# Optimization experiments

Measured on AMD Instinct MI355X. Metric: run time of the kernel, lower is better.

## Reference

```python
import jax, jax.numpy as jnp
import numpy as np

U, I, D = 50000, 100000, 64
N = U + I
B = 8192
E_UI = 1_000_000   # directed user->item edges, symmetrized to 2M
E_U = 500_000      # per user metapath graph
E_I = 1_000_000    # per item metapath graph
SA_HID = 128


def _seg_sum(data, idx, n):
    return jax.ops.segment_sum(data, idx, num_segments=n)


def gcn_spmm(edges, x):
    """scipy-style symmetric normalization: D^-1/2 A D^-1/2 x, inf->0."""
    n = x.shape[0]
    row, col = edges[0], edges[1]
    deg = _seg_sum(jnp.ones(row.shape, x.dtype), row, n)  # symmetric adj
    dinv = jnp.where(deg > 0, 1.0 / jnp.sqrt(jnp.maximum(deg, 1e-12)), 0.0)
    msg = x[col] * dinv[col][:, None]          # [E, D] gather
    return _seg_sum(msg, row, n) * dinv[:, None]


def graph_conv(edges, x):
    """DGL GraphConv(norm='both', weight=None, bias=None): degrees clamped min 1."""
    n = x.shape[0]
    src, dst = edges[0], edges[1]
    ones = jnp.ones(src.shape, x.dtype)
    dout = jnp.maximum(_seg_sum(ones, src, n), 1.0)
    din = jnp.maximum(_seg_sum(ones, dst, n), 1.0)
    msg = x[src] * (1.0 / jnp.sqrt(dout))[src][:, None]
    return _seg_sum(msg, dst, n) * (1.0 / jnp.sqrt(din))[:, None]


def han_layer(x, e1, e2, W1, b1, w2):
    # per-metapath GraphConv, stack -> [N, M=2, D]
    z = jnp.stack([graph_conv(e1, x), graph_conv(e2, x)], axis=1)
    w = jnp.tanh(z @ W1 + b1) @ w2            # [N, 2, 1]
    beta = jax.nn.softmax(w.mean(0), axis=0)  # [2, 1]
    return (beta[None, :, :] * z).sum(1)      # [N, D]


def setup_inputs() -> dict:
    key = jax.random.key(0)
    ks = jax.random.split(key, 16)
    user_feat = jax.random.normal(ks[0], (U, D), jnp.float32) * 0.1
    item_feat = jax.random.normal(ks[1], (I, D), jnp.float32) * 0.1
    sa_u_W1 = jax.random.normal(ks[2], (D, SA_HID), jnp.float32) * (1.0 / np.sqrt(D))
    sa_u_b1 = jnp.zeros((SA_HID,), jnp.float32)
    sa_u_w2 = jax.random.normal(ks[3], (SA_HID, 1), jnp.float32) * (1.0 / np.sqrt(SA_HID))
    sa_i_W1 = jax.random.normal(ks[4], (D, SA_HID), jnp.float32) * (1.0 / np.sqrt(D))
    sa_i_b1 = jnp.zeros((SA_HID,), jnp.float32)
    sa_i_w2 = jax.random.normal(ks[5], (SA_HID, 1), jnp.float32) * (1.0 / np.sqrt(SA_HID))
    # symmetric bipartite user-item adjacency over N global nodes
    r = jax.random.randint(ks[6], (E_UI,), 0, U, jnp.int32)
    c = jax.random.randint(ks[7], (E_UI,), U, N, jnp.int32)
    ui_edges = jnp.stack([jnp.concatenate([r, c]), jnp.concatenate([c, r])])  # [2, 2E]
    u_edges1 = jax.random.randint(ks[8], (2, E_U), 0, U, jnp.int32)
    u_edges2 = jax.random.randint(ks[9], (2, E_U), 0, U, jnp.int32)
    i_edges1 = jax.random.randint(ks[10], (2, E_I), 0, I, jnp.int32)
    i_edges2 = jax.random.randint(ks[11], (2, E_I), 0, I, jnp.int32)
    user_idx = jax.random.randint(ks[12], (B,), 0, U, jnp.int32)
    item_idx = jax.random.randint(ks[13], (B,), 0, I, jnp.int32)
    neg_item_idx = jax.random.randint(ks[14], (B,), 0, B, jnp.int32)
    return dict(user_feat=user_feat, item_feat=item_feat,
                sa_u_W1=sa_u_W1, sa_u_b1=sa_u_b1, sa_u_w2=sa_u_w2,
                sa_i_W1=sa_i_W1, sa_i_b1=sa_i_b1, sa_i_w2=sa_i_w2,
                ui_edges=ui_edges, u_edges1=u_edges1, u_edges2=u_edges2,
                i_edges1=i_edges1, i_edges2=i_edges2,
                user_idx=user_idx, item_idx=item_idx, neg_item_idx=neg_item_idx)


def reference(user_feat, item_feat, sa_u_W1, sa_u_b1, sa_u_w2,
              sa_i_W1, sa_i_b1, sa_i_w2, ui_edges, u_edges1, u_edges2,
              i_edges1, i_edges2, user_idx, item_idx, neg_item_idx):
    ui = jnp.concatenate([user_feat, item_feat], axis=0)  # [N, D]
    hu, hi = user_feat, item_feat
    for _ in range(2):
        ui = gcn_spmm(ui_edges, ui)
        hu = han_layer(hu, u_edges1, u_edges2, sa_u_W1, sa_u_b1, sa_u_w2)
        hi = han_layer(hi, i_edges1, i_edges2, sa_i_W1, sa_i_b1, sa_i_w2)
    user_all = 0.5 * hu + 0.5 * ui[:U]
    item_all = 0.5 * hi + 0.5 * ui[U:]
    user_emb = user_all[user_idx]
    item_emb = item_all[item_idx]
    neg_item_feat = item_emb[neg_item_idx]
    return (user_emb, item_emb, neg_item_feat)
```

## Files before the change

kernel.cpp:

```cpp
#include <hip/hip_runtime.h>
#include <hip/hip_bf16.h>
#include <stdint.h>

typedef long long ll;
typedef unsigned short ushort_t;
typedef __attribute__((ext_vector_type(8))) short bf16x8;
typedef __attribute__((ext_vector_type(4))) float f32x4;

static inline int cdiv_ll(ll a, ll b) { return (int)((a + b - 1) / b); }

#define BIN_SHIFT 8
#define BIN_SIZE 256
#define KMAX 3072
#define BT 1024
#define FILL_CAP 7936

__global__ void k_detect(const unsigned int* __restrict__ dw, const ll n_dw, int* __restrict__ flag) {
    __shared__ int sc[256];
    int tid = threadIdx.x;
    int cnt = 0;
    for (int s = 0; s < 32; s++) {
        ll idx = (ll)(s * 256 + tid);
        ll i = (idx * n_dw) / 8192;
        unsigned v = dw[i];
        unsigned lo = v & 0xFFFFu;
        unsigned ex = (lo >> 7) & 0xFFu;
        bool pl = (lo == 0u) || (lo == 0x8000u) || (ex >= 0x60u && ex <= 0x8Fu);
        cnt += pl ? 1 : 0;
    }
    sc[tid] = cnt;
    __syncthreads();
    for (int o = 128; o > 0; o >>= 1) { if (tid < o) sc[tid] += sc[tid + o]; __syncthreads(); }
    if (tid == 0) *flag = (sc[0] * 2 > 8192) ? 1 : 0;
}

__device__ __forceinline__ float load_in(const void* p, ll i, int isbf16) {
    if (isbf16) return __bfloat162float(((const __hip_bfloat16*)p)[i]);
    return ((const float*)p)[i];
}

__device__ __forceinline__ float bf2f(ushort_t u) {
    return __uint_as_float(((unsigned)u) << 16);
}
__device__ __forceinline__ ushort_t f2bf(float f) {
    unsigned u = __float_as_uint(f);
    unsigned r = (u + 0x7FFFu + ((u >> 16) & 1u)) >> 16;
    return (ushort_t)r;
}

__global__ void k_cvt_weights(const void* __restrict__ W1u, const void* __restrict__ b1u,
                              const void* __restrict__ w2u, const void* __restrict__ W1i,
                              const void* __restrict__ b1i, const void* __restrict__ w2i,
                              ushort_t* __restrict__ Wbu, float* __restrict__ fb1u,
                              float* __restrict__ fw2u, ushort_t* __restrict__ Wbi,
                              float* __restrict__ fb1i, float* __restrict__ fw2i,
                              const int* __restrict__ flag) {
    int i = blockIdx.x * blockDim.x + threadIdx.x;
    int bf = *flag;
    const int WSZ = 64 * 128;
    if (i < WSZ) {
        int d = i >> 7, h = i & 127;
        Wbu[h * 64 + d] = f2bf(load_in(W1u, i, bf));
    } else if (i < WSZ + 128) {
        fb1u[i - WSZ] = load_in(b1u, i - WSZ, bf);
    } else if (i < WSZ + 256) {
        fw2u[i - WSZ - 128] = load_in(w2u, i - WSZ - 128, bf);
    } else if (i < 2 * WSZ + 256) {
        int j = i - WSZ - 256;
        int d = j >> 7, h = j & 127;
        Wbi[h * 64 + d] = f2bf(load_in(W1i, j, bf));
    } else if (i < 2 * WSZ + 384) {
        fb1i[i - 2 * WSZ - 256] = load_in(b1i, i - 2 * WSZ - 256, bf);
    } else if (i < 2 * WSZ + 512) {
        fw2i[i - 2 * WSZ - 384] = load_in(w2i, i - 2 * WSZ - 384, bf);
    }
}

__device__ __forceinline__ void decode_rec(ll t,
    const int* __restrict__ uiR, const int* __restrict__ uiC,
    const int* __restrict__ u1s, const int* __restrict__ u1d,
    const int* __restrict__ u2s, const int* __restrict__ u2d,
    const int* __restrict__ i1s, const int* __restrict__ i1d,
    const int* __restrict__ i2s, const int* __restrict__ i2d,
    const ll E2, const ll EU1, const ll EU2, const ll EI1, const ll EI2,
    const int N, const int U, const int I, const int M,
    int& key, int& col) {
    if (t < E2) { key = uiR[t]; col = uiC[t]; return; }
    t -= E2;
    if (t < EU1) { key = N + u1d[t]; col = u1s[t]; return; }
    t -= EU1;
    if (t < EU1) { key = M + u1s[t]; col = 0; return; }
    t -= EU1;
    if (t < EU2) { key = N + U + u2d[t]; col = u2s[t]; return; }
    t -= EU2;
    if (t < EU2) { key = M + U + u2s[t]; col = 0; return; }
    t -= EU2;
    if (t < EI1) { key = N + 2 * U + i1d[t]; col = i1s[t]; return; }
    t -= EI1;
    if (t < EI1) { key = M + 2 * U + i1s[t]; col = 0; return; }
    t -= EI1;
    if (t < EI2) { key = N + 2 * U + I + i2d[t]; col = i2s[t]; return; }
    t -= EI2;
    key = M + 2 * U + I + i2s[t]; col = 0;
}

__device__ __forceinline__ int decode_key(ll t,
    const int* __restrict__ uiR,
    const int* __restrict__ u1s, const int* __restrict__ u1d,
    const int* __restrict__ u2s, const int* __restrict__ u2d,
    const int* __restrict__ i1s, const int* __restrict__ i1d,
    const int* __restrict__ i2s, const int* __restrict__ i2d,
    const ll E2, const ll EU1, const ll EU2, const ll EI1, const ll EI2,
    const int N, const int U, const int I, const int M) {
    if (t < E2) return uiR[t];
    t -= E2;
    if (t < EU1) return N + u1d[t];
    t -= EU1;
    if (t < EU1) return M + u1s[t];
    t -= EU1;
    if (t < EU2) return N + U + u2d[t];
    t -= EU2;
    if (t < EU2) return M + U + u2s[t];
    t -= EU2;
    if (t < EI1) return N + 2 * U + i1d[t];
    t -= EI1;
    if (t < EI1) return M + 2 * U + i1s[t];
    t -= EI1;
    if (t < EI2) return N + 2 * U + I + i2d[t];
    t -= EI2;
    return M + 2 * U + I + i2s[t];
}

#define DECODE_ARGS uiR, uiC, u1s, u1d, u2s, u2d, i1s, i1d, i2s, i2d, \
                    E2, EU1, EU2, EI1, EI2, N, U, I, M

__global__ __launch_bounds__(BT) void kA_hist(
    const int* __restrict__ uiR,
    const int* __restrict__ u1s, const int* __restrict__ u1d,
    const int* __restrict__ u2s, const int* __restrict__ u2d,
    const int* __restrict__ i1s, const int* __restrict__ i1d,
    const int* __restrict__ i2s, const int* __restrict__ i2d,
    const ll E2, const ll EU1, const ll EU2, const ll EI1, const ll EI2,
    const int N, const int U, const int I, const int M,
    const ll RT, const ll CHUNKD, const int K,
    int* __restrict__ btot ,
    int* __restrict__ whist ) {
    __shared__ int hist[KMAX];
    for (int i = threadIdx.x; i < K; i += BT) hist[i] = 0;
    __syncthreads();
    ll base = (ll)blockIdx.x * CHUNKD;
    ll lim = base + CHUNKD;
    if (lim > RT) lim = RT;
    for (ll t = base + threadIdx.x; t < lim; t += BT) {
        int key = decode_key(t, uiR, u1s, u1d, u2s, u2d, i1s, i1d, i2s, i2d,
                             E2, EU1, EU2, EI1, EI2, N, U, I, M);
        atomicAdd(&hist[key >> BIN_SHIFT], 1);
    }
    __syncthreads();
    ll wb = (ll)blockIdx.x * K;
    for (int k = threadIdx.x; k < K; k += BT) {
        int h = hist[k];
        whist[wb + k] = h;
        if (h) atomicAdd(&btot[k * 32], h);
    }
}

__global__ __launch_bounds__(1024) void k_bscan(const int* __restrict__ btot,
                                                int* __restrict__ bbase,
                                                int* __restrict__ bcursor, const int K) {
    __shared__ int sh[1024];
    __shared__ int carry;
    int t = threadIdx.x;
    if (t == 0) carry = 0;
    __syncthreads();
    for (int base = 0; base < K; base += 1024) {
        int idx = base + t;
        int v = (idx < K) ? btot[idx * 32] : 0;
        sh[t] = v;
        __syncthreads();
        for (int off = 1; off < 1024; off <<= 1) {
            int x = (t >= off) ? sh[t - off] : 0;
            __syncthreads();
            sh[t] += x;
            __syncthreads();
        }
        if (idx < K) {
            int ex = carry + sh[t] - v;
            bbase[idx] = ex;
            bcursor[idx * 32] = ex;
        }
        __syncthreads();
        if (t == 0) carry += sh[1023];
        __syncthreads();
    }
}

__global__ __launch_bounds__(BT) void kA_scatter(
    const int* __restrict__ uiR, const int* __restrict__ uiC,
    const int* __restrict__ u1s, const int* __restrict__ u1d,
    const int* __restrict__ u2s, const int* __restrict__ u2d,
    const int* __restrict__ i1s, const int* __restrict__ i1d,
    const int* __restrict__ i2s, const int* __restrict__ i2d,
    const ll E2, const ll EU1, const ll EU2, const ll EI1, const ll EI2,
    const int N, const int U, const int I, const int M,
    const ll RT, const ll CHUNKD, const int K, int* __restrict__ bcursor,
    const int* __restrict__ whist,
    unsigned* __restrict__ binned) {
    __shared__ int lcur[KMAX];
    ll wb = (ll)blockIdx.x * K;
    for (int k = threadIdx.x; k < K; k += BT) {
        int h = whist[wb + k];
        lcur[k] = h ? atomicAdd(&bcursor[k * 32], h) : 0;
    }
    __syncthreads();
    ll base = (ll)blockIdx.x * CHUNKD;
    ll lim = base + CHUNKD;
    if (lim > RT) lim = RT;
    for (ll t = base + threadIdx.x; t < lim; t += BT) {
        int key, col;
        decode_rec(t, DECODE_ARGS, key, col);
        int pos = atomicAdd(&lcur[key >> BIN_SHIFT], 1);
        binned[pos] = ((unsigned)(key & 255) << 24) | (unsigned)col;
    }
}

__global__ __launch_bounds__(256) void kB1_count(const unsigned* __restrict__ binned,
                                                 const int* __restrict__ bbase,
                                                 const int* __restrict__ btot,
                                                 int* __restrict__ counts, const int M2) {
    __shared__ int cnt[BIN_SIZE];
    int b = blockIdx.x;
    int lo = b << BIN_SHIFT;
    int hi = min(lo + BIN_SIZE, M2);
    for (int i = threadIdx.x; i < BIN_SIZE; i += 256) cnt[i] = 0;
    __syncthreads();
    int s = bbase[b], n = btot[b * 32];
    for (int j = s + threadIdx.x; j < s + n; j += 256) {
        atomicAdd(&cnt[binned[j] >> 24], 1);
    }
    __syncthreads();
    for (int i = threadIdx.x; i < hi - lo; i += 256) counts[lo + i] = cnt[i];
}

__global__ void k_norm_all(const int* __restrict__ counts, float* __restrict__ nrm,
                           const int N, const int total) {
    int i = blockIdx.x * blockDim.x + threadIdx.x;
    if (i < total) {
        int c = counts[i];
        if (i < N) nrm[i] = (c > 0) ? (1.0f / sqrtf((float)c)) : 0.0f;
        else nrm[i] = 1.0f / sqrtf(fmaxf((float)c, 1.0f));
    }
}

#define SCAN_T 256
#define SCAN_ELEMS 8
#define SCAN_CHUNK (SCAN_T * SCAN_ELEMS)

__global__ __launch_bounds__(256) void k_scanA(const int* __restrict__ in, const int n,
                                               int* __restrict__ out, int* __restrict__ bsum) {
    __shared__ int sh[SCAN_T];
    int t = threadIdx.x;
    ll base = (ll)blockIdx.x * SCAN_CHUNK + (ll)t * SCAN_ELEMS;
    int v[SCAN_ELEMS];
    int tot = 0;
#pragma unroll
    for (int k = 0; k < SCAN_ELEMS; k++) {
        ll i = base + k;
        v[k] = (i < n) ? in[i] : 0;
        tot += v[k];
    }
    sh[t] = tot;
    __syncthreads();
    for (int off = 1; off < SCAN_T; off <<= 1) {
        int x = (t >= off) ? sh[t - off] : 0;
        __syncthreads();
        sh[t] += x;
        __syncthreads();
    }
    int run = sh[t] - tot;
#pragma unroll
    for (int k = 0; k < SCAN_ELEMS; k++) {
        ll i = base + k;
        if (i < n) out[i] = run;
        run += v[k];
    }
    if (t == SCAN_T - 1) bsum[blockIdx.x] = sh[SCAN_T - 1];
}

__global__ __launch_bounds__(256) void k_scanB(int* __restrict__ bsum, const int nb) {
    __shared__ int sh[256];
    int t = threadIdx.x;
    int running = 0;
    for (int base = 0; base < nb; base += 256) {
        int idx = base + t;
        int v = (idx < nb) ? bsum[idx] : 0;
        sh[t] = v;
        __syncthreads();
        for (int off = 1; off < 256; off <<= 1) {
            int x = (t >= off) ? sh[t - off] : 0;
            __syncthreads();
            sh[t] += x;
            __syncthreads();
        }
        if (idx < nb) bsum[idx] = running + sh[t] - v;
        int tot = sh[255];
        __syncthreads();
        running += tot;
    }
}

__global__ void k_scanC(int* __restrict__ S, const int n, const int* __restrict__ bsum, const int ET) {
    ll i = (ll)blockIdx.x * blockDim.x + threadIdx.x;
    if (i < n) S[i] += bsum[i / SCAN_CHUNK];
    if (i == 0) S[n] = ET;
}

__global__ __launch_bounds__(256) void kB2_fill(const unsigned* __restrict__ binned,
                                                const int* __restrict__ bbase,
                                                const int* __restrict__ btot,
                                                const int* __restrict__ S,
                                                const float* __restrict__ nrm,
                                                const int N, const int U, const int I,
                                                const int M,
                                                int2* __restrict__ ev_all) {
    __shared__ int scur[BIN_SIZE];
    __shared__ int2 buf[FILL_CAP];
    int b = blockIdx.x;
    int lo = b << BIN_SHIFT;
    int hi = min(lo + BIN_SIZE, M);
    int obase = S[lo];
    int nfill = S[hi] - obase;
    int s = bbase[b], n = btot[b * 32];
    const int segU = N + U, seg2U = N + 2 * U, segI = N + 2 * U + I;
    if (n <= FILL_CAP) {
        for (int i = threadIdx.x; i < hi - lo; i += 256) scur[i] = S[lo + i] - obase;
        __syncthreads();
        for (int j = s + threadIdx.x; j < s + n; j += 256) {
            unsigned rec = binned[j];
            int key = lo + (int)(rec >> 24);
            if (key < M) {
                int pos = atomicAdd(&scur[key - lo], 1);
                int col = (int)(rec & 0xFFFFFFu);
                int nidx;
                if (key < N)          nidx = col;
                else if (key < segU)  nidx = M + col;
                else if (key < seg2U) nidx = M + U + col;
                else if (key < segI)  nidx = M + 2 * U + col;
                else                  nidx = M + 2 * U + I + col;
                buf[pos] = make_int2(col * 64, __float_as_int(nrm[nidx]));
            }
        }
        __syncthreads();
        for (int i = threadIdx.x; i < nfill; i += 256)
            ev_all[obase + i] = buf[i];
    } else {
        for (int i = threadIdx.x; i < hi - lo; i += 256) scur[i] = S[lo + i];
        __syncthreads();
        for (int j = s + threadIdx.x; j < s + n; j += 256) {
            unsigned rec = binned[j];
            int key = lo + (int)(rec >> 24);
            if (key < M) {
                int pos = atomicAdd(&scur[key - lo], 1);
                int col = (int)(rec & 0xFFFFFFu);
                int nidx;
                if (key < N)          nidx = col;
                else if (key < segU)  nidx = M + col;
                else if (key < seg2U) nidx = M + U + col;
                else if (key < segI)  nidx = M + 2 * U + col;
                else                  nidx = M + 2 * U + I + col;
                ev_all[pos] = make_int2(col * 64, __float_as_int(nrm[nidx]));
            }
        }
    }
}

__global__ void k_init(const void* __restrict__ uf, const void* __restrict__ itf,
                       ushort_t* __restrict__ ui, ushort_t* __restrict__ hu,
                       ushort_t* __restrict__ hi,
                       const ll nu64, const ll ntot64, const int* __restrict__ flag) {
    ll t = (ll)blockIdx.x * blockDim.x + threadIdx.x;
    int bf = *flag;
    if (t < nu64) {
        ushort_t v = bf ? ((const ushort_t*)uf)[t] : f2bf(((const float*)uf)[t]);
        ui[t] = v; hu[t] = v;
    } else if (t < ntot64) {
        ll j = t - nu64;
        ushort_t v = bf ? ((const ushort_t*)itf)[j] : f2bf(((const float*)itf)[j]);
        ui[t] = v; hi[j] = v;
    }
}

typedef __attribute__((ext_vector_type(4))) unsigned short ushort4v;

__global__ __launch_bounds__(256) void k_gather5(const int* __restrict__ S,
                                                 const int2* __restrict__ ev,
                                                 const float* __restrict__ nrm,
                                                 const ushort_t* __restrict__ xui,
                                                 const ushort_t* __restrict__ xu,
                                                 const ushort_t* __restrict__ xi,
                                                 ushort_t* __restrict__ out_ui,
                                                 ushort_t* __restrict__ o_zu1,
                                                 ushort_t* __restrict__ o_zu2,
                                                 ushort_t* __restrict__ o_zi1,
                                                 ushort_t* __restrict__ o_zi2,
                                                 const int N, const int U, const int I,
                                                 const int M) {
    ll gt = (ll)blockIdx.x * blockDim.x + threadIdx.x;
    int w = (int)(gt >> 4);
    int l16 = threadIdx.x & 15;
    if (w >= M) return;
    const ushort_t* x;
    ushort_t* out;
    int orow;
    if (w < N)                  { x = xui; out = out_ui; orow = w; }
    else if (w < N + U)         { x = xu;  out = o_zu1;  orow = w - N; }
    else if (w < N + 2 * U)     { x = xu;  out = o_zu2;  orow = w - N - U; }
    else if (w < N + 2 * U + I) { x = xi;  out = o_zi1;  orow = w - N - 2 * U; }
    else                        { x = xi;  out = o_zi2;  orow = w - N - 2 * U - I; }
    int s = S[w], e = S[w + 1];
    float a0 = 0.0f, a1 = 0.0f, a2 = 0.0f, a3 = 0.0f;
    unsigned doff = (unsigned)(l16 * 4);
    for (int j = s; j < e; j += 8) {
#pragma unroll
        for (int k = 0; k < 8; k++) {
            int jj = j + k;
            bool live = jj < e;
            int2 pr = ev[live ? jj : s];
            float nn = live ? __int_as_float(pr.y) : 0.0f;
            unsigned off = (unsigned)pr.x + doff;
            ushort4v xv = *(const ushort4v*)&x[off];
            a0 += bf2f(xv.x) * nn;
            a1 += bf2f(xv.y) * nn;
            a2 += bf2f(xv.z) * nn;
            a3 += bf2f(xv.w) * nn;
        }
    }
    float rn = nrm[w];
    ushort4v o;
    o.x = f2bf(a0 * rn); o.y = f2bf(a1 * rn);
    o.z = f2bf(a2 * rn); o.w = f2bf(a3 * rn);
    *(ushort4v*)&out[(ll)orow * 64 + doff] = o;
}

__device__ __forceinline__ float fast_tanh(float x) {
    return 1.0f - 2.0f / (__expf(2.0f * x) + 1.0f);
}

__global__ __launch_bounds__(256) void k_attn2(const ushort_t* __restrict__ zu1,
                                               const ushort_t* __restrict__ zu2,
                                               const ushort_t* __restrict__ Wbu,
                                               const float* __restrict__ b1u,
                                               const float* __restrict__ w2u,
                                               const int nU, float* __restrict__ wsU,
                                               const ushort_t* __restrict__ zi1,
                                               const ushort_t* __restrict__ zi2,
                                               const ushort_t* __restrict__ Wbi,
                                               const float* __restrict__ b1f_i,
                                               const float* __restrict__ w2f_i,
                                               const int nI, float* __restrict__ wsI,
                                               const int half) {
    __shared__ float red0[4], red1[4];
    bool isU = (int)blockIdx.x < half;
    const ushort_t* z1 = isU ? zu1 : zi1;
    const ushort_t* z2 = isU ? zu2 : zi2;
    const ushort_t* Wb = isU ? Wbu : Wbi;
    const float* b1f = isU ? b1u : b1f_i;
    const float* w2f = isU ? w2u : w2f_i;
    const int n = isU ? nU : nI;
    float* wsum = isU ? wsU : wsI;
    int blk = isU ? (int)blockIdx.x : (int)blockIdx.x - half;

    int tid = threadIdx.x;
    int lane = tid & 63;
    int wid = tid >> 6;
    int col = lane & 15;
    int quad = lane >> 4;

    bf16x8 wb[8][2];
#pragma unroll
    for (int ht = 0; ht < 8; ht++) {
        int h = ht * 16 + col;
#pragma unroll
        for (int ks = 0; ks < 2; ks++) {
            wb[ht][ks] = *(const bf16x8*)&Wb[h * 64 + ks * 32 + quad * 8];
        }
    }
    float b1v[8], w2v[8];
#pragma unroll
    for (int ht = 0; ht < 8; ht++) {
        b1v[ht] = b1f[ht * 16 + col];
        w2v[ht] = w2f[ht * 16 + col];
    }

    float w0 = 0.0f, w1 = 0.0f;
    int ntiles = (n + 15) >> 4;
    int gw = blk * 4 + wid;
    int nw = half * 4;
    const bf16x8 zero8 = {0, 0, 0, 0, 0, 0, 0, 0};

    for (int tile = gw; tile < ntiles; tile += nw) {
        int nodeA = tile * 16 + col;
        bool va = nodeA < n;
        bf16x8 a1[2], a2[2];
#pragma unroll
        for (int ks = 0; ks < 2; ks++) {
            const bf16x8* p1 = (const bf16x8*)&z1[(ll)nodeA * 64 + ks * 32 + quad * 8];
            const bf16x8* p2 = (const bf16x8*)&z2[(ll)nodeA * 64 + ks * 32 + quad * 8];
            a1[ks] = va ? p1[0] : zero8;
            a2[ks] = va ? p2[0] : zero8;
        }
#pragma unroll
        for (int ht = 0; ht < 8; ht++) {
            f32x4 c1 = {0.f, 0.f, 0.f, 0.f};
            f32x4 c2 = {0.f, 0.f, 0.f, 0.f};
            c1 = __builtin_amdgcn_mfma_f32_16x16x32_bf16(a1[0], wb[ht][0], c1, 0, 0, 0);
            c1 = __builtin_amdgcn_mfma_f32_16x16x32_bf16(a1[1], wb[ht][1], c1, 0, 0, 0);
            c2 = __builtin_amdgcn_mfma_f32_16x16x32_bf16(a2[0], wb[ht][0], c2, 0, 0, 0);
            c2 = __builtin_amdgcn_mfma_f32_16x16x32_bf16(a2[1], wb[ht][1], c2, 0, 0, 0);
#pragma unroll
            for (int r = 0; r < 4; r++) {
                int node_row = tile * 16 + quad * 4 + r;
                bool vr = node_row < n;
                float t1 = fast_tanh(c1[r] + b1v[ht]) * w2v[ht];
                float t2 = fast_tanh(c2[r] + b1v[ht]) * w2v[ht];
                w0 += vr ? t1 : 0.0f;
                w1 += vr ? t2 : 0.0f;
            }
        }
    }

    for (int off = 32; off > 0; off >>= 1) {
        w0 += __shfl_down(w0, off);
        w1 += __shfl_down(w1, off);
    }
    if (lane == 0) { red0[wid] = w0; red1[wid] = w1; }
    __syncthreads();
    if (tid == 0) {
        atomicAdd(&wsum[0], red0[0] + red0[1] + red0[2] + red0[3]);
        atomicAdd(&wsum[1], red1[0] + red1[1] + red1[2] + red1[3]);
    }
}

__global__ void k_combine2(const ushort_t* __restrict__ zu1, const ushort_t* __restrict__ zu2,
                           const float* __restrict__ wsU, const float inv_nU,
                           ushort_t* __restrict__ hu, const ll nu64,
                           const ushort_t* __restrict__ zi1, const ushort_t* __restrict__ zi2,
                           const float* __restrict__ wsI, const float inv_nI,
                           ushort_t* __restrict__ hi, const ll ntot64) {
    ll t = (ll)blockIdx.x * blockDim.x + threadIdx.x;
    if (t < nu64) {
        float m0 = wsU[0] * inv_nU, m1 = wsU[1] * inv_nU;
        float mx = fmaxf(m0, m1);
        float e0 = __expf(m0 - mx), e1 = __expf(m1 - mx);
        float inv_s = 1.0f / (e0 + e1);
        hu[t] = f2bf((e0 * bf2f(zu1[t]) + e1 * bf2f(zu2[t])) * inv_s);
    } else if (t < ntot64) {
        ll j = t - nu64;
        float m0 = wsI[0] * inv_nI, m1 = wsI[1] * inv_nI;
        float mx = fmaxf(m0, m1);
        float e0 = __expf(m0 - mx), e1 = __expf(m1 - mx);
        float inv_s = 1.0f / (e0 + e1);
        hi[j] = f2bf((e0 * bf2f(zi1[j]) + e1 * bf2f(zi2[j])) * inv_s);
    }
}

__device__ __forceinline__ void store_out(void* out, ll i, float v, int isbf16) {
    if (isbf16) ((ushort_t*)out)[i] = f2bf(v);
    else ((float*)out)[i] = v;
}

__global__ void k_out(const ushort_t* __restrict__ hu, const ushort_t* __restrict__ hi,
                      const ushort_t* __restrict__ ui, const int* __restrict__ user_idx,
                      const int* __restrict__ item_idx, const int* __restrict__ neg_idx,
                      void* __restrict__ out, const int B, const ll U,
                      const int* __restrict__ flag) {
    ll t = (ll)blockIdx.x * blockDim.x + threadIdx.x;
    int bf = *flag;
    int d = (int)(t & 63);
    ll b = t >> 6;
    if (b < B) {
        int u = user_idx[b];
        float v = 0.5f * bf2f(hu[(ll)u * 64 + d]) + 0.5f * bf2f(ui[(ll)u * 64 + d]);
        store_out(out, b * 64 + d, v, bf);
    } else if (b < 2 * (ll)B) {
        ll bb = b - B;
        int it = item_idx[bb];
        float v = 0.5f * bf2f(hi[(ll)it * 64 + d]) + 0.5f * bf2f(ui[(U + it) * 64 + d]);
        store_out(out, (ll)B * 64 + bb * 64 + d, v, bf);
    } else if (b < 3 * (ll)B) {
        ll bb = b - 2 * (ll)B;
        int it = item_idx[neg_idx[bb]];
        float v = 0.5f * bf2f(hi[(ll)it * 64 + d]) + 0.5f * bf2f(ui[(U + it) * 64 + d]);
        store_out(out, (ll)2 * B * 64 + bb * 64 + d, v, bf);
    }
}

extern "C" void kernel_launch(void* const* d_in, const int* in_sizes, int n_in,
                              void* d_out, int out_size, void* d_ws, size_t ws_size,
                              hipStream_t stream) {
    const int D = 64;
    const ll U = in_sizes[0] / D;
    const ll I = in_sizes[1] / D;
    const ll N = U + I;
    const ll E2  = in_sizes[8] / 2;
    const ll EU1 = in_sizes[9] / 2;
    const ll EU2 = in_sizes[10] / 2;
    const ll EI1 = in_sizes[11] / 2;
    const ll EI2 = in_sizes[12] / 2;
    const ll ET = E2 + EU1 + EU2 + EI1 + EI2;
    const ll RT = E2 + 2 * (EU1 + EU2 + EI1 + EI2);
    const int B = in_sizes[13];
    const int M = (int)(N + 2 * U + 2 * I);
    const int M2 = (int)(N + 4 * U + 4 * I);
    const int K = (M2 + BIN_SIZE - 1) >> BIN_SHIFT;
    const int KM = (M + BIN_SIZE - 1) >> BIN_SHIFT;
    if (K > KMAX) return;

    const void* user_feat = d_in[0];
    const void* item_feat = d_in[1];
    const int* uiR = (const int*)d_in[8];
    const int* uiC = uiR + E2;
    const int* u1s = (const int*)d_in[9];
    const int* u1d = u1s + EU1;
    const int* u2s = (const int*)d_in[10];
    const int* u2d = u2s + EU2;
    const int* i1s = (const int*)d_in[11];
    const int* i1d = i1s + EI1;
    const int* i2s = (const int*)d_in[12];
    const int* i2d = i2s + EI2;
    const int* user_idx = (const int*)d_in[13];
    const int* item_idx = (const int*)d_in[14];
    const int* neg_idx  = (const int*)d_in[15];

    const int T = 256;
    const ll CHUNKD = ((RT + 251) / 252 + (ll)BT - 1) / (ll)BT * (ll)BT;
    const int nWG_A = cdiv_ll(RT, CHUNKD);

    ushort_t* q = (ushort_t*)d_ws;
    ushort_t* ui0 = q; q += N * 64;
    ushort_t* ui1 = q; q += N * 64;
    ushort_t* zi1 = q; q += I * 64;
    ushort_t* zi2 = q; q += I * 64;
    ushort_t* zu1 = q; q += U * 64;
    ushort_t* zu2 = q; q += U * 64;
    ushort_t* hu  = q; q += U * 64;
    ushort_t* hi  = q; q += I * 64;
    size_t feat_bytes = (size_t)(q - (ushort_t*)d_ws) * 2;
    if (feat_bytes < (size_t)RT * 4) return;
    unsigned* binned = (unsigned*)d_ws;

    float* p = (float*)(((uintptr_t)q + 15) & ~(uintptr_t)15);
    float* nrm = p;  p += M2;
    ushort_t* Wbu = (ushort_t*)p; p += 64 * 128 / 2;
    ushort_t* Wbi = (ushort_t*)p; p += 64 * 128 / 2;
    float* wb1u = p; p += 128;
    float* ww2u = p; p += 128;
    float* wb1i = p; p += 128;
    float* ww2i = p; p += 128;
    float* scratch = p; p += 16;

    int* ip = (int*)p;
    int* btot = ip;    ip += KMAX * 32;
    int* bbase = ip;   ip += KMAX;
    int* bcursor = ip; ip += KMAX * 32;
    int* counts = ip;  ip += M2;
    int* S = ip;       ip += M + 1;
    ip = (int*)(((uintptr_t)ip + 7) & ~(uintptr_t)7);
    int2* ev_all = (int2*)ip; ip += 2 * ET;
    int* whist = ip;   ip += (size_t)nWG_A * K;
    int* bsum = ip;    ip += 256;
    int* flag = ip;    ip += 4;
    size_t needed = (size_t)((char*)ip - (char*)d_ws);
    if (ws_size < needed) return;

    k_detect<<<1, 256, 0, stream>>>((const unsigned int*)user_feat, (ll)in_sizes[0] / 2, flag);
    k_cvt_weights<<<cdiv_ll(2 * (64 * 128 + 256), T), T, 0, stream>>>(
        d_in[2], d_in[3], d_in[4], d_in[5], d_in[6], d_in[7],
        Wbu, wb1u, ww2u, Wbi, wb1i, ww2i, flag);

    hipMemsetAsync(btot, 0, (size_t)KMAX * 32 * sizeof(int), stream);
    hipMemsetAsync(scratch, 0, 16 * sizeof(float), stream);
    kA_hist<<<nWG_A, BT, 0, stream>>>(uiR, u1s, u1d, u2s, u2d, i1s, i1d, i2s, i2d,
                                      E2, EU1, EU2, EI1, EI2, (int)N, (int)U, (int)I, M,
                                      RT, CHUNKD, K, btot, whist);
    k_bscan<<<1, 1024, 0, stream>>>(btot, bbase, bcursor, K);
    kA_scatter<<<nWG_A, BT, 0, stream>>>(uiR, uiC, u1s, u1d, u2s, u2d, i1s, i1d, i2s, i2d,
                                         E2, EU1, EU2, EI1, EI2, (int)N, (int)U, (int)I, M,
                                         RT, CHUNKD, K, bcursor, whist, binned);
    kB1_count<<<K, T, 0, stream>>>(binned, bbase, btot, counts, M2);
    k_norm_all<<<cdiv_ll(M2, T), T, 0, stream>>>(counts, nrm, (int)N, M2);
    {
        int nb = (M + SCAN_CHUNK - 1) / SCAN_CHUNK;
        k_scanA<<<nb, SCAN_T, 0, stream>>>(counts, M, S, bsum);
        k_scanB<<<1, 256, 0, stream>>>(bsum, nb);
        k_scanC<<<cdiv_ll(M, T), T, 0, stream>>>(S, M, bsum, (int)ET);
    }
    kB2_fill<<<KM, T, 0, stream>>>(binned, bbase, btot, S, nrm,
                                   (int)N, (int)U, (int)I, M, ev_all);

    k_init<<<cdiv_ll(N * 64, T), T, 0, stream>>>(user_feat, item_feat, ui0, hu, hi, U * 64, N * 64, flag);

    ushort_t* uiA = ui0;
    ushort_t* uiB = ui1;
    const int ATTN_HALF = 512;

    for (int layer = 0; layer < 2; layer++) {
        float* wsU = scratch + (layer ? 8 : 0);
        float* wsI = scratch + (layer ? 12 : 4);

        k_gather5<<<cdiv_ll((ll)M * 16, T), T, 0, stream>>>(
            S, ev_all, nrm, uiA, hu, hi,
            uiB, zu1, zu2, zi1, zi2,
            (int)N, (int)U, (int)I, M);
        { ushort_t* tmp = uiA; uiA = uiB; uiB = tmp; }

        k_attn2<<<2 * ATTN_HALF, T, 0, stream>>>(
            zu1, zu2, Wbu, wb1u, ww2u, (int)U, wsU,
            zi1, zi2, Wbi, wb1i, ww2i, (int)I, wsI, ATTN_HALF);

        k_combine2<<<cdiv_ll((U + I) * 64, T), T, 0, stream>>>(
            zu1, zu2, wsU, 1.0f / (float)U, hu, U * 64,
            zi1, zi2, wsI, 1.0f / (float)I, hi, (U + I) * 64);
    }

    k_out<<<cdiv_ll((ll)3 * B * 64, T), T, 0, stream>>>(hu, hi, uiA, user_idx, item_idx, neg_idx,
                                                        d_out, B, U, flag);
}
```

Before: 737.8 us.

## Use 4 lanes per row with 16-wide bf16 vectors in gather SpMM

The gather kernel now assigns 4 threads per output row instead of 16, each loading two 16-byte bf16x8 vectors and accumulating 16 features, with the inner unroll reduced from 8 to 2 edges. This cuts redundant per-lane edge-index loads and loop overhead and uses wider memory transactions. The cost is more registers per thread and fewer lanes per row, so load balance across rows with uneven degrees may suffer and latency hiding may drop. Separately, the binning chunk-size divisor changes from 252 to 506, creating more workgroups in the binning stage.

```diff
diff --git a/kernel.cpp b/kernel.cpp
--- a/kernel.cpp
+++ b/kernel.cpp
@@ -390,8 +390,6 @@
     }
 }
 
-typedef __attribute__((ext_vector_type(4))) unsigned short ushort4v;
-
 __global__ __launch_bounds__(256) void k_gather5(const int* __restrict__ S,
                                                  const int2* __restrict__ ev,
                                                  const float* __restrict__ nrm,
@@ -406,8 +404,8 @@
                                                  const int N, const int U, const int I,
                                                  const int M) {
     ll gt = (ll)blockIdx.x * blockDim.x + threadIdx.x;
-    int w = (int)(gt >> 4);
-    int l16 = threadIdx.x & 15;
+    int w = (int)(gt >> 2);
+    int l4 = threadIdx.x & 3;
     if (w >= M) return;
     const ushort_t* x;
     ushort_t* out;
@@ -418,28 +416,34 @@
     else if (w < N + 2 * U + I) { x = xi;  out = o_zi1;  orow = w - N - 2 * U; }
     else                        { x = xi;  out = o_zi2;  orow = w - N - 2 * U - I; }
     int s = S[w], e = S[w + 1];
-    float a0 = 0.0f, a1 = 0.0f, a2 = 0.0f, a3 = 0.0f;
-    unsigned doff = (unsigned)(l16 * 4);
-    for (int j = s; j < e; j += 8) {
-#pragma unroll
-        for (int k = 0; k < 8; k++) {
+    float a[16];
+#pragma unroll
+    for (int i = 0; i < 16; i++) a[i] = 0.0f;
+    unsigned doff = (unsigned)(l4 * 16);
+    for (int j = s; j < e; j += 2) {
+#pragma unroll
+        for (int k = 0; k < 2; k++) {
             int jj = j + k;
             bool live = jj < e;
             int2 pr = ev[live ? jj : s];
             float nn = live ? __int_as_float(pr.y) : 0.0f;
             unsigned off = (unsigned)pr.x + doff;
-            ushort4v xv = *(const ushort4v*)&x[off];
-            a0 += bf2f(xv.x) * nn;
-            a1 += bf2f(xv.y) * nn;
-            a2 += bf2f(xv.z) * nn;
-            a3 += bf2f(xv.w) * nn;
+            bf16x8 x0 = *(const bf16x8*)&x[off];
+            bf16x8 x1 = *(const bf16x8*)&x[off + 8];
+#pragma unroll
+            for (int i = 0; i < 8; i++) a[i]     += bf2f((ushort_t)x0[i]) * nn;
+#pragma unroll
+            for (int i = 0; i < 8; i++) a[8 + i] += bf2f((ushort_t)x1[i]) * nn;
         }
     }
     float rn = nrm[w];
-    ushort4v o;
-    o.x = f2bf(a0 * rn); o.y = f2bf(a1 * rn);
-    o.z = f2bf(a2 * rn); o.w = f2bf(a3 * rn);
-    *(ushort4v*)&out[(ll)orow * 64 + doff] = o;
+    bf16x8 o0, o1;
+#pragma unroll
+    for (int i = 0; i < 8; i++) o0[i] = (short)f2bf(a[i] * rn);
+#pragma unroll
+    for (int i = 0; i < 8; i++) o1[i] = (short)f2bf(a[8 + i] * rn);
+    *(bf16x8*)&out[(ll)orow * 64 + doff] = o0;
+    *(bf16x8*)&out[(ll)orow * 64 + doff + 8] = o1;
 }
 
 __device__ __forceinline__ float fast_tanh(float x) {
@@ -633,7 +637,7 @@
     const int* neg_idx  = (const int*)d_in[15];
 
     const int T = 256;
-    const ll CHUNKD = ((RT + 251) / 252 + (ll)BT - 1) / (ll)BT * (ll)BT;
+    const ll CHUNKD = ((RT + 505) / 506 + (ll)BT - 1) / (ll)BT * (ll)BT;
     const int nWG_A = cdiv_ll(RT, CHUNKD);
 
     ushort_t* q = (ushort_t*)d_ws;
@@ -708,7 +712,7 @@
         float* wsU = scratch + (layer ? 8 : 0);
         float* wsI = scratch + (layer ? 12 : 4);
 
-        k_gather5<<<cdiv_ll((ll)M * 16, T), T, 0, stream>>>(
+        k_gather5<<<cdiv_ll((ll)M * 4, T), T, 0, stream>>>(
             S, ev_all, nrm, uiA, hu, hi,
             uiB, zu1, zu2, zi1, zi2,
             (int)N, (int)U, (int)I, M);
```

New measurement: 661.3 us. 10.4% less time.
